# Optimization experiments

Hardware: AMD Instinct MI355X
Metric: run time of the kernel (lower is better)

Reference implementation:

```python
import jax, jax.numpy as jnp
import numpy as np

DIM = 1024
SCALE = 1.0 / np.sqrt(DIM).astype(np.float32)


def setup_inputs() -> dict:
    key = jax.random.key(0)
    ks = jax.random.split(key, 8)
    B, S, D = 4, 2048, DIM
    x = jax.random.normal(ks[0], (B, S, D), dtype=jnp.float32)
    mask = jnp.zeros((S, S), dtype=jnp.float32)  # additive mask, broadcast over batch
    # learned params (nn.Linear: y = x @ W.T + b); store W already transposed for x @ W
    init = 1.0 / np.sqrt(D)
    Wq = jax.random.uniform(ks[1], (D, D), jnp.float32, -init, init)
    bq = jax.random.uniform(ks[2], (D,), jnp.float32, -init, init)
    Wk = jax.random.uniform(ks[3], (D, D), jnp.float32, -init, init)
    bk = jax.random.uniform(ks[4], (D,), jnp.float32, -init, init)
    Wv = jax.random.uniform(ks[5], (D, D), jnp.float32, -init, init)
    bv = jax.random.uniform(ks[6], (D,), jnp.float32, -init, init)
    return {"x": x, "mask": mask, "Wq": Wq, "bq": bq, "Wk": Wk, "bk": bk, "Wv": Wv, "bv": bv}


def reference(x, mask, Wq, bq, Wk, bk, Wv, bv):
    # single-head full-dim attention, scaled by 1/sqrt(dim) (as in the source)
    q = x @ Wq + bq                      # [B, S, D]
    k = x @ Wk + bk                      # [B, S, D]
    v = x @ Wv + bv                      # [B, S, D]
    scores = jnp.einsum('bqd,bkd->bqk', q, k) * SCALE  # [B, S, S]
    scores = scores + mask               # additive mask, broadcast
    attn = jax.nn.softmax(scores, axis=-1)
    # dropout(p=0.1) is identity in eval mode
    return jnp.einsum('bqk,bkd->bqd', attn, v)  # [B, S, D]
```

## Files before the change

### kernel.cpp

```cpp
#include <hip/hip_runtime.h>

typedef unsigned short u16;
typedef unsigned int u32;

typedef __attribute__((ext_vector_type(8))) short bf16x8;
typedef __attribute__((ext_vector_type(4))) float f32x4;

static __device__ __forceinline__ u16 f2bf(float f) {
    u32 u = __float_as_uint(f);
    u32 r = (u + 0x7FFFu + ((u >> 16) & 1u)) >> 16;
    return (u16)r;
}
static __device__ __forceinline__ float bf2f(u16 h) {
    return __uint_as_float(((u32)h) << 16);
}
static __device__ __forceinline__ u32 pack2(float a, float b) {
    return (u32)f2bf(a) | ((u32)f2bf(b) << 16);
}

__global__ __launch_bounds__(256) void prep_kernel(
    const float* __restrict__ x, u16* __restrict__ xb,
    const float* __restrict__ mask, u16* __restrict__ maskb,
    const float* __restrict__ Wq, const float* __restrict__ Wk, const float* __restrict__ Wv,
    u16* __restrict__ T0, u16* __restrict__ T1, u16* __restrict__ T2,
    const float* __restrict__ bq, const float* __restrict__ bk,
    float* __restrict__ bqk, float* __restrict__ rsum) {
    const int D = 1024;
    int bid = blockIdx.x;
    const int tid = threadIdx.x;
    if (bid < 8192) {
        long i = (long)bid * 256 + tid;
        float4 v = ((const float4*)x)[i];
        ushort4 o; o.x = f2bf(v.x); o.y = f2bf(v.y); o.z = f2bf(v.z); o.w = f2bf(v.w);
        ((ushort4*)xb)[i] = o;
        return;
    }
    bid -= 8192;
    if (bid < 4096) {
        long i = (long)bid * 256 + tid;
        float4 v = ((const float4*)mask)[i];
        ushort4 o; o.x = f2bf(v.x); o.y = f2bf(v.y); o.z = f2bf(v.z); o.w = f2bf(v.w);
        ((ushort4*)maskb)[i] = o;
        return;
    }
    bid -= 4096;
    if (bid < 3072) {
        __shared__ float t[32][33];
        const int z = bid >> 10, loc = bid & 1023;
        const int bx = loc & 31, by = loc >> 5;
        const float* W = (z == 0) ? Wq : (z == 1) ? Wk : Wv;
        u16* WT = (z == 0) ? T0 : (z == 1) ? T1 : T2;
        const int tx = tid & 31, ty = tid >> 5;
#pragma unroll
        for (int i = ty; i < 32; i += 8)
            t[i][tx] = W[(long)(by * 32 + i) * D + bx * 32 + tx];
        __syncthreads();
#pragma unroll
        for (int i = ty; i < 32; i += 8)
            WT[(long)(bx * 32 + i) * D + by * 32 + tx] = f2bf(t[tx][i]);
        return;
    }
    bid -= 3072;
    if (bid < 8) {
        int i = bid * 256 + tid;
        bqk[i] = (i < 1024) ? bq[i] : bk[i - 1024];
        return;
    }
    bid -= 8;
    rsum[bid * 256 + tid] = 0.f;
}

static __device__ __forceinline__ void gemm_core(
    u16* __restrict__ SM,
    const u16* __restrict__ Ab, int lda,
    const u16* __restrict__ Bb, int ldb,
    void* __restrict__ Cb, int ldc, int c_bf16,
    const float* __restrict__ bias, int bias_mode,
    const u16* __restrict__ madd, int mask_ld,
    float* __restrict__ rowsum, int rs_mode,
    float scale, int K, int tm, int tn) {
    const int tid = threadIdx.x, wave = tid >> 6, lane = tid & 63;
    const int wm = (wave >> 1) * 64, wn = (wave & 1) * 64;
    const int lr = lane >> 2, c = lane & 3;
    const int fm = lane & 15, fq = lane >> 4;

    f32x4 acc[4][4];
#pragma unroll
    for (int i = 0; i < 4; i++)
#pragma unroll
        for (int j = 0; j < 4; j++) acc[i][j] = (f32x4){0.f, 0.f, 0.f, 0.f};

    const int T = K >> 5;

    auto stage = [&](int t, int buf) {
        u16* As = SM + buf * 8192;
        u16* Bs = As + 4096;
#pragma unroll
        for (int r = 0; r < 2; r++) {
            const int rl = r * 64 + wave * 16;
            const int row = rl + lr;
            const int kc = (t << 5) + ((c ^ ((row ^ (row >> 2)) & 3)) << 3);
            const u16* ga = Ab + (long)(tm + row) * lda + kc;
            const u16* gb = Bb + (long)(tn + row) * ldb + kc;
            __builtin_amdgcn_global_load_lds((const __attribute__((address_space(1))) void*)ga,
                                             (__attribute__((address_space(3))) void*)&As[rl * 32],
                                             16, 0, 0);
            __builtin_amdgcn_global_load_lds((const __attribute__((address_space(1))) void*)gb,
                                             (__attribute__((address_space(3))) void*)&Bs[rl * 32],
                                             16, 0, 0);
        }
    };

    stage(0, 0);
    __syncthreads();
    for (int t = 0; t < T; t++) {
        const int cur = t & 1;
        if (t + 1 < T) stage(t + 1, cur ^ 1);
        const u16* As = SM + cur * 8192;
        const u16* Bs = As + 4096;
        bf16x8 af[4], bfr[4];
#pragma unroll
        for (int i = 0; i < 4; i++) {
            int row = wm + i * 16 + fm;
            af[i] = *(const bf16x8*)&As[row * 32 + ((fq ^ ((row ^ (row >> 2)) & 3)) << 3)];
        }
#pragma unroll
        for (int j = 0; j < 4; j++) {
            int row = wn + j * 16 + fm;
            bfr[j] = *(const bf16x8*)&Bs[row * 32 + ((fq ^ ((row ^ (row >> 2)) & 3)) << 3)];
        }
#pragma unroll
        for (int i = 0; i < 4; i++)
#pragma unroll
            for (int j = 0; j < 4; j++)
                acc[i][j] = __builtin_amdgcn_mfma_f32_16x16x32_bf16(af[i], bfr[j], acc[i][j], 0, 0, 0);
        if (t + 1 < T) __syncthreads();
    }
    __syncthreads();

    float* EP = (float*)SM + wave * 1088;
    const int row16 = lane >> 2, cb = (lane & 3) * 16;
    float4 bc[4];
    if (bias_mode == 1) {
#pragma unroll
        for (int q = 0; q < 4; q++) bc[q] = *(const float4*)&bias[tn + wn + cb + q * 4];
    }
#pragma unroll
    for (int i = 0; i < 4; i++) {
#pragma unroll
        for (int j = 0; j < 4; j++)
#pragma unroll
            for (int r = 0; r < 4; r++)
                EP[(fq * 4 + r) * 68 + j * 16 + fm] = acc[i][j][r];
        const long grow = tm + wm + i * 16 + row16;
        float rb = (bias_mode == 2) ? bias[grow] : 0.f;
        float4 t4[4];
#pragma unroll
        for (int q = 0; q < 4; q++) {
            float4 v = *(const float4*)&EP[row16 * 68 + cb + q * 4];
            v.x = v.x * scale + rb; v.y = v.y * scale + rb;
            v.z = v.z * scale + rb; v.w = v.w * scale + rb;
            if (bias_mode == 1) { v.x += bc[q].x; v.y += bc[q].y; v.z += bc[q].z; v.w += bc[q].w; }
            if (madd) {
                ushort4 m4 = *(const ushort4*)&madd[grow * mask_ld + tn + wn + cb + q * 4];
                v.x += bf2f(m4.x); v.y += bf2f(m4.y); v.z += bf2f(m4.z); v.w += bf2f(m4.w);
            }
            t4[q] = v;
        }
        if (rs_mode == 1) {
            float s = 0.f;
#pragma unroll
            for (int q = 0; q < 4; q++) {
                t4[q].x = __expf(t4[q].x); t4[q].y = __expf(t4[q].y);
                t4[q].z = __expf(t4[q].z); t4[q].w = __expf(t4[q].w);
                s += t4[q].x + t4[q].y + t4[q].z + t4[q].w;
            }
            s += __shfl_xor(s, 1);
            s += __shfl_xor(s, 2);
            if ((lane & 3) == 0) atomicAdd(&rowsum[grow], s);
        } else if (rs_mode == 2) {
            float inv = 1.f / rowsum[grow];
#pragma unroll
            for (int q = 0; q < 4; q++) {
                t4[q].x *= inv; t4[q].y *= inv; t4[q].z *= inv; t4[q].w *= inv;
            }
        }
        if (c_bf16) {
            u16* dst = (u16*)Cb + grow * ldc + tn + wn + cb;
            uint4 o0 = {pack2(t4[0].x, t4[0].y), pack2(t4[0].z, t4[0].w),
                        pack2(t4[1].x, t4[1].y), pack2(t4[1].z, t4[1].w)};
            uint4 o1 = {pack2(t4[2].x, t4[2].y), pack2(t4[2].z, t4[2].w),
                        pack2(t4[3].x, t4[3].y), pack2(t4[3].z, t4[3].w)};
            *(uint4*)dst = o0;
            *(uint4*)(dst + 8) = o1;
        } else {
            float* dst = (float*)Cb + grow * ldc + tn + wn + cb;
#pragma unroll
            for (int q = 0; q < 4; q++) *(float4*)(dst + q * 4) = t4[q];
        }
    }
}

__global__ __launch_bounds__(256, 4) void gemm_qkvt_kernel(
    const u16* __restrict__ xb, const u16* __restrict__ wqkt, const u16* __restrict__ wvt,
    u16* __restrict__ QK, u16* __restrict__ VT,
    const float* __restrict__ bqk, const float* __restrict__ bv) {
    __shared__ __align__(16) u16 SM[2][256 * 32];
    const int D = 1024, MS = 8192;
    const int id = blockIdx.x;
    if (id < 1024) {
        gemm_core(&SM[0][0], xb, D, wqkt, D, QK, 2 * D, 1, bqk, 1, nullptr, 0,
                  nullptr, 0, 1.0f, D, (id >> 4) * 128, (id & 15) * 128);
    } else {
        const int f = id - 1024;
        gemm_core(&SM[0][0], wvt, D, xb, D, VT, MS, 1, bv, 2, nullptr, 0,
                  nullptr, 0, 1.0f, D, (f >> 6) * 128, (f & 63) * 128);
    }
}

__global__ __launch_bounds__(256, 4) void gemm_sc_kernel(
    const u16* __restrict__ QK, u16* __restrict__ sc,
    const u16* __restrict__ maskb, float* __restrict__ rsum, float scale) {
    __shared__ __align__(16) u16 SM[2][256 * 32];
    const int S = 2048, D = 1024;
    const int lin = blockIdx.x;
    const int xcd = lin & 7, r = lin >> 3;
    const int bx = r & 15, ylo = (r >> 4) & 7;
    const int bz = xcd >> 1, by = (xcd & 1) * 8 + ylo;
    gemm_core(&SM[0][0],
              QK + (long)bz * S * 2 * D, 2 * D,
              QK + D + (long)bz * S * 2 * D, 2 * D,
              sc + (long)bz * S * S, S, 1, nullptr, 0,
              maskb, S, rsum + (long)bz * S, 1,
              scale, D, by * 128, bx * 128);
}

__global__ __launch_bounds__(256, 4) void gemm_pv_kernel(
    const u16* __restrict__ sc, const u16* __restrict__ VT,
    float* __restrict__ out, const float* __restrict__ rsum) {
    __shared__ __align__(16) u16 SM[2][256 * 32];
    const int S = 2048, D = 1024, MS = 8192;
    const int xcd = blockIdx.x;
    const int s = blockIdx.y + 16 * blockIdx.z;
    const int bz = xcd >> 1;
    const int byi = (xcd & 1) * 8 + (s >> 3);
    const int bxi = s & 7;
    gemm_core(&SM[0][0],
              sc + (long)bz * S * S, S,
              VT + (long)bz * S, MS,
              out + (long)bz * S * D, D, 0, nullptr, 0,
              nullptr, 0, (float*)(rsum + (long)bz * S), 2,
              1.0f, S, byi * 128, bxi * 128);
}

extern "C" void kernel_launch(void* const* d_in, const int* in_sizes, int n_in,
                              void* d_out, int out_size, void* d_ws, size_t ws_size,
                              hipStream_t stream) {
    const float* x    = (const float*)d_in[0];
    const float* mask = (const float*)d_in[1];
    const float* Wq   = (const float*)d_in[2];
    const float* bq   = (const float*)d_in[3];
    const float* Wk   = (const float*)d_in[4];
    const float* bk   = (const float*)d_in[5];
    const float* Wv   = (const float*)d_in[6];
    const float* bv   = (const float*)d_in[7];
    float* out = (float*)d_out;

    const int B = 4, S = 2048, D = 1024;
    const long MS = (long)B * S;

    size_t need = (size_t)MS * D * 2 + (size_t)(2 * D) * D * 2 + (size_t)D * D * 2
                + (size_t)(2 * D) * 4 + (size_t)MS * (2 * D) * 2 + (size_t)D * MS * 2
                + (size_t)B * S * S * 2 + (size_t)B * S * 4 + (size_t)S * S * 2;
    if (ws_size < need) return;

    char* ws = (char*)d_ws;
    u16*  xb   = (u16*)ws;  ws += (long)MS * D * 2;
    u16*  wqkt = (u16*)ws;  ws += (long)(2 * D) * D * 2;
    u16*  wvt  = (u16*)ws;  ws += (long)D * D * 2;
    float* bqk = (float*)ws; ws += (long)(2 * D) * 4;
    u16*  QK   = (u16*)ws;  ws += (long)MS * (2 * D) * 2;
    u16*  VT   = (u16*)ws;  ws += (long)D * MS * 2;
    u16*  sc   = (u16*)ws;  ws += (long)B * S * S * 2;
    float* rsum = (float*)ws; ws += (long)B * S * 4;
    u16*  maskb = (u16*)ws; ws += (long)S * S * 2;

    const float SCALE = 0.03125f;

    prep_kernel<<<15400, 256, 0, stream>>>(x, xb, mask, maskb, Wq, Wk, Wv,
                                           wqkt, wqkt + (long)D * D, wvt,
                                           bq, bk, bqk, rsum);
    gemm_qkvt_kernel<<<1536, 256, 0, stream>>>(xb, wqkt, wvt, QK, VT, bqk, bv);
    gemm_sc_kernel<<<1024, 256, 0, stream>>>(QK, sc, maskb, rsum, SCALE);
    gemm_pv_kernel<<<dim3(8, 16, 4), 256, 0, stream>>>(sc, VT, out, rsum);
}
```

Before: 277.5 us.

## Load MFMA fragments directly from global memory in score and PV GEMMs

Replaces the LDS-staged, double-buffered GEMM main loop in the score and PV kernels with a register double-buffered loop that loads bf16x8 MFMA fragments straight from global memory. Each lane does per-row 16-byte loads that depend on L2/L1 for reuse, and occupancy hints drop to 2 blocks. The mask conversion and rowsum zeroing move out of the prep kernel into extra blocks of the QKV GEMM launch. This removes LDS traffic and barriers, but global loads become less coalesced and reuse across waves now depends on the cache hierarchy.

After: 417.0 us. 1.5x slower.

```diff
diff --git a/kernel.cpp b/kernel.cpp
--- a/kernel.cpp
+++ b/kernel.cpp
@@ -20,11 +20,10 @@
 
 __global__ __launch_bounds__(256) void prep_kernel(
     const float* __restrict__ x, u16* __restrict__ xb,
-    const float* __restrict__ mask, u16* __restrict__ maskb,
     const float* __restrict__ Wq, const float* __restrict__ Wk, const float* __restrict__ Wv,
     u16* __restrict__ T0, u16* __restrict__ T1, u16* __restrict__ T2,
     const float* __restrict__ bq, const float* __restrict__ bk,
-    float* __restrict__ bqk, float* __restrict__ rsum) {
+    float* __restrict__ bqk) {
     const int D = 1024;
     int bid = blockIdx.x;
     const int tid = threadIdx.x;
@@ -36,14 +35,6 @@
         return;
     }
     bid -= 8192;
-    if (bid < 4096) {
-        long i = (long)bid * 256 + tid;
-        float4 v = ((const float4*)mask)[i];
-        ushort4 o; o.x = f2bf(v.x); o.y = f2bf(v.y); o.z = f2bf(v.z); o.w = f2bf(v.w);
-        ((ushort4*)maskb)[i] = o;
-        return;
-    }
-    bid -= 4096;
     if (bid < 3072) {
         __shared__ float t[32][33];
         const int z = bid >> 10, loc = bid & 1023;
@@ -61,13 +52,10 @@
         return;
     }
     bid -= 3072;
-    if (bid < 8) {
+    {
         int i = bid * 256 + tid;
         bqk[i] = (i < 1024) ? bq[i] : bk[i - 1024];
-        return;
-    }
-    bid -= 8;
-    rsum[bid * 256 + tid] = 0.f;
+    }
 }
 
 static __device__ __forceinline__ void gemm_core(
@@ -76,8 +64,6 @@
     const u16* __restrict__ Bb, int ldb,
     void* __restrict__ Cb, int ldc, int c_bf16,
     const float* __restrict__ bias, int bias_mode,
-    const u16* __restrict__ madd, int mask_ld,
-    float* __restrict__ rowsum, int rs_mode,
     float scale, int K, int tm, int tn) {
     const int tid = threadIdx.x, wave = tid >> 6, lane = tid & 63;
     const int wm = (wave >> 1) * 64, wn = (wave & 1) * 64;
@@ -161,96 +147,201 @@
             v.x = v.x * scale + rb; v.y = v.y * scale + rb;
             v.z = v.z * scale + rb; v.w = v.w * scale + rb;
             if (bias_mode == 1) { v.x += bc[q].x; v.y += bc[q].y; v.z += bc[q].z; v.w += bc[q].w; }
-            if (madd) {
-                ushort4 m4 = *(const ushort4*)&madd[grow * mask_ld + tn + wn + cb + q * 4];
-                v.x += bf2f(m4.x); v.y += bf2f(m4.y); v.z += bf2f(m4.z); v.w += bf2f(m4.w);
-            }
             t4[q] = v;
         }
-        if (rs_mode == 1) {
-            float s = 0.f;
-#pragma unroll
-            for (int q = 0; q < 4; q++) {
-                t4[q].x = __expf(t4[q].x); t4[q].y = __expf(t4[q].y);
-                t4[q].z = __expf(t4[q].z); t4[q].w = __expf(t4[q].w);
-                s += t4[q].x + t4[q].y + t4[q].z + t4[q].w;
-            }
-            s += __shfl_xor(s, 1);
-            s += __shfl_xor(s, 2);
-            if ((lane & 3) == 0) atomicAdd(&rowsum[grow], s);
-        } else if (rs_mode == 2) {
-            float inv = 1.f / rowsum[grow];
-#pragma unroll
-            for (int q = 0; q < 4; q++) {
-                t4[q].x *= inv; t4[q].y *= inv; t4[q].z *= inv; t4[q].w *= inv;
-            }
-        }
-        if (c_bf16) {
-            u16* dst = (u16*)Cb + grow * ldc + tn + wn + cb;
-            uint4 o0 = {pack2(t4[0].x, t4[0].y), pack2(t4[0].z, t4[0].w),
-                        pack2(t4[1].x, t4[1].y), pack2(t4[1].z, t4[1].w)};
-            uint4 o1 = {pack2(t4[2].x, t4[2].y), pack2(t4[2].z, t4[2].w),
-                        pack2(t4[3].x, t4[3].y), pack2(t4[3].z, t4[3].w)};
-            *(uint4*)dst = o0;
-            *(uint4*)(dst + 8) = o1;
-        } else {
-            float* dst = (float*)Cb + grow * ldc + tn + wn + cb;
-#pragma unroll
-            for (int q = 0; q < 4; q++) *(float4*)(dst + q * 4) = t4[q];
-        }
+        u16* dst = (u16*)Cb + grow * ldc + tn + wn + cb;
+        uint4 o0 = {pack2(t4[0].x, t4[0].y), pack2(t4[0].z, t4[0].w),
+                    pack2(t4[1].x, t4[1].y), pack2(t4[1].z, t4[1].w)};
+        uint4 o1 = {pack2(t4[2].x, t4[2].y), pack2(t4[2].z, t4[2].w),
+                    pack2(t4[3].x, t4[3].y), pack2(t4[3].z, t4[3].w)};
+        *(uint4*)dst = o0;
+        *(uint4*)(dst + 8) = o1;
     }
 }
 
 __global__ __launch_bounds__(256, 4) void gemm_qkvt_kernel(
     const u16* __restrict__ xb, const u16* __restrict__ wqkt, const u16* __restrict__ wvt,
     u16* __restrict__ QK, u16* __restrict__ VT,
-    const float* __restrict__ bqk, const float* __restrict__ bv) {
+    const float* __restrict__ bqk, const float* __restrict__ bv,
+    const float* __restrict__ mask, u16* __restrict__ maskb, float* __restrict__ rsum) {
     __shared__ __align__(16) u16 SM[2][256 * 32];
     const int D = 1024, MS = 8192;
     const int id = blockIdx.x;
     if (id < 1024) {
-        gemm_core(&SM[0][0], xb, D, wqkt, D, QK, 2 * D, 1, bqk, 1, nullptr, 0,
-                  nullptr, 0, 1.0f, D, (id >> 4) * 128, (id & 15) * 128);
+        gemm_core(&SM[0][0], xb, D, wqkt, D, QK, 2 * D, 1, bqk, 1,
+                  1.0f, D, (id >> 4) * 128, (id & 15) * 128);
+    } else if (id < 1536) {
+        const int f = id - 1024;
+        gemm_core(&SM[0][0], wvt, D, xb, D, VT, MS, 1, bv, 2,
+                  1.0f, D, (f >> 6) * 128, (f & 63) * 128);
+    } else if (id < 5632) {
+        long i = (long)(id - 1536) * 256 + threadIdx.x;
+        float4 v = ((const float4*)mask)[i];
+        ushort4 o; o.x = f2bf(v.x); o.y = f2bf(v.y); o.z = f2bf(v.z); o.w = f2bf(v.w);
+        ((ushort4*)maskb)[i] = o;
     } else {
-        const int f = id - 1024;
-        gemm_core(&SM[0][0], wvt, D, xb, D, VT, MS, 1, bv, 2, nullptr, 0,
-                  nullptr, 0, 1.0f, D, (f >> 6) * 128, (f & 63) * 128);
-    }
-}
-
-__global__ __launch_bounds__(256, 4) void gemm_sc_kernel(
+        rsum[(id - 5632) * 256 + threadIdx.x] = 0.f;
+    }
+}
+
+static __device__ __forceinline__ void gemm_direct_loop(
+    const u16* __restrict__ Ab, int lda,
+    const u16* __restrict__ Bb, int ldb,
+    int tm, int tn, int K, f32x4 (&acc)[4][4]) {
+    const int tid = threadIdx.x, wave = tid >> 6, lane = tid & 63;
+    const int wm = (wave >> 1) * 64, wn = (wave & 1) * 64;
+    const int fm = lane & 15, fq = lane >> 4;
+    const int T = K >> 5;
+
+    const u16* Ap = Ab + (long)(tm + wm + fm) * lda + fq * 8;
+    const u16* Bp = Bb + (long)(tn + wn + fm) * ldb + fq * 8;
+
+    bf16x8 a0[4], b0[4], a1[4], b1[4];
+#pragma unroll
+    for (int i = 0; i < 4; i++) {
+        a0[i] = *(const bf16x8*)(Ap + (long)i * 16 * lda);
+        b0[i] = *(const bf16x8*)(Bp + (long)i * 16 * ldb);
+    }
+    for (int t = 0; t < T; t += 2) {
+        if (t + 1 < T) {
+#pragma unroll
+            for (int i = 0; i < 4; i++) {
+                a1[i] = *(const bf16x8*)(Ap + (long)i * 16 * lda + (t + 1) * 32);
+                b1[i] = *(const bf16x8*)(Bp + (long)i * 16 * ldb + (t + 1) * 32);
+            }
+        }
+#pragma unroll
+        for (int i = 0; i < 4; i++)
+#pragma unroll
+            for (int j = 0; j < 4; j++)
+                acc[i][j] = __builtin_amdgcn_mfma_f32_16x16x32_bf16(a0[i], b0[j], acc[i][j], 0, 0, 0);
+        if (t + 2 < T) {
+#pragma unroll
+            for (int i = 0; i < 4; i++) {
+                a0[i] = *(const bf16x8*)(Ap + (long)i * 16 * lda + (t + 2) * 32);
+                b0[i] = *(const bf16x8*)(Bp + (long)i * 16 * ldb + (t + 2) * 32);
+            }
+        }
+        if (t + 1 < T) {
+#pragma unroll
+            for (int i = 0; i < 4; i++)
+#pragma unroll
+                for (int j = 0; j < 4; j++)
+                    acc[i][j] = __builtin_amdgcn_mfma_f32_16x16x32_bf16(a1[i], b1[j], acc[i][j], 0, 0, 0);
+        }
+    }
+}
+
+__global__ __launch_bounds__(256, 2) void sc_direct_kernel(
     const u16* __restrict__ QK, u16* __restrict__ sc,
     const u16* __restrict__ maskb, float* __restrict__ rsum, float scale) {
-    __shared__ __align__(16) u16 SM[2][256 * 32];
+    __shared__ __align__(16) float EPS[4 * 1088];
     const int S = 2048, D = 1024;
     const int lin = blockIdx.x;
     const int xcd = lin & 7, r = lin >> 3;
     const int bx = r & 15, ylo = (r >> 4) & 7;
     const int bz = xcd >> 1, by = (xcd & 1) * 8 + ylo;
-    gemm_core(&SM[0][0],
-              QK + (long)bz * S * 2 * D, 2 * D,
-              QK + D + (long)bz * S * 2 * D, 2 * D,
-              sc + (long)bz * S * S, S, 1, nullptr, 0,
-              maskb, S, rsum + (long)bz * S, 1,
-              scale, D, by * 128, bx * 128);
-}
-
-__global__ __launch_bounds__(256, 4) void gemm_pv_kernel(
+    const int tm = by * 128, tn = bx * 128;
+    const u16* Ab = QK + (long)bz * S * 2 * D;
+    const u16* Bb = Ab + D;
+    u16* Cb = sc + (long)bz * S * S;
+    float* rs = rsum + (long)bz * S;
+
+    f32x4 acc[4][4];
+#pragma unroll
+    for (int i = 0; i < 4; i++)
+#pragma unroll
+        for (int j = 0; j < 4; j++) acc[i][j] = (f32x4){0.f, 0.f, 0.f, 0.f};
+
+    gemm_direct_loop(Ab, 2 * D, Bb, 2 * D, tm, tn, D, acc);
+
+    const int tid = threadIdx.x, wave = tid >> 6, lane = tid & 63;
+    const int wm = (wave >> 1) * 64, wn = (wave & 1) * 64;
+    const int fm = lane & 15, fq = lane >> 4;
+    float* EP = EPS + wave * 1088;
+    const int row16 = lane >> 2, cb = (lane & 3) * 16;
+#pragma unroll
+    for (int i = 0; i < 4; i++) {
+#pragma unroll
+        for (int j = 0; j < 4; j++)
+#pragma unroll
+            for (int rr = 0; rr < 4; rr++)
+                EP[(fq * 4 + rr) * 68 + j * 16 + fm] = acc[i][j][rr];
+        const long grow = tm + wm + i * 16 + row16;
+        float4 t4[4];
+#pragma unroll
+        for (int q = 0; q < 4; q++) {
+            float4 v = *(const float4*)&EP[row16 * 68 + cb + q * 4];
+            ushort4 m4 = *(const ushort4*)&maskb[grow * S + tn + wn + cb + q * 4];
+            v.x = v.x * scale + bf2f(m4.x); v.y = v.y * scale + bf2f(m4.y);
+            v.z = v.z * scale + bf2f(m4.z); v.w = v.w * scale + bf2f(m4.w);
+            t4[q] = v;
+        }
+        float s = 0.f;
+#pragma unroll
+        for (int q = 0; q < 4; q++) {
+            t4[q].x = __expf(t4[q].x); t4[q].y = __expf(t4[q].y);
+            t4[q].z = __expf(t4[q].z); t4[q].w = __expf(t4[q].w);
+            s += t4[q].x + t4[q].y + t4[q].z + t4[q].w;
+        }
+        s += __shfl_xor(s, 1);
+        s += __shfl_xor(s, 2);
+        if ((lane & 3) == 0) atomicAdd(&rs[grow], s);
+        u16* dst = Cb + grow * S + tn + wn + cb;
+        uint4 o0 = {pack2(t4[0].x, t4[0].y), pack2(t4[0].z, t4[0].w),
+                    pack2(t4[1].x, t4[1].y), pack2(t4[1].z, t4[1].w)};
+        uint4 o1 = {pack2(t4[2].x, t4[2].y), pack2(t4[2].z, t4[2].w),
+                    pack2(t4[3].x, t4[3].y), pack2(t4[3].z, t4[3].w)};
+        *(uint4*)dst = o0;
+        *(uint4*)(dst + 8) = o1;
+    }
+}
+
+__global__ __launch_bounds__(256, 2) void pv_direct_kernel(
     const u16* __restrict__ sc, const u16* __restrict__ VT,
     float* __restrict__ out, const float* __restrict__ rsum) {
-    __shared__ __align__(16) u16 SM[2][256 * 32];
+    __shared__ __align__(16) float EPS[4 * 1088];
     const int S = 2048, D = 1024, MS = 8192;
     const int xcd = blockIdx.x;
-    const int s = blockIdx.y + 16 * blockIdx.z;
+    const int s = blockIdx.y + gridDim.y * blockIdx.z;
     const int bz = xcd >> 1;
     const int byi = (xcd & 1) * 8 + (s >> 3);
     const int bxi = s & 7;
-    gemm_core(&SM[0][0],
-              sc + (long)bz * S * S, S,
-              VT + (long)bz * S, MS,
-              out + (long)bz * S * D, D, 0, nullptr, 0,
-              nullptr, 0, (float*)(rsum + (long)bz * S), 2,
-              1.0f, S, byi * 128, bxi * 128);
+    const int tm = byi * 128, tn = bxi * 128;
+    const u16* Ab = sc + (long)bz * S * S;
+    const u16* Bb = VT + (long)bz * S;
+    const float* rs = rsum + (long)bz * S;
+
+    f32x4 acc[4][4];
+#pragma unroll
+    for (int i = 0; i < 4; i++)
+#pragma unroll
+        for (int j = 0; j < 4; j++) acc[i][j] = (f32x4){0.f, 0.f, 0.f, 0.f};
+
+    gemm_direct_loop(Ab, S, Bb, MS, tm, tn, S, acc);
+
+    const int tid = threadIdx.x, wave = tid >> 6, lane = tid & 63;
+    const int wm = (wave >> 1) * 64, wn = (wave & 1) * 64;
+    const int fm = lane & 15, fq = lane >> 4;
+    float* EP = EPS + wave * 1088;
+    const int row16 = lane >> 2, cb = (lane & 3) * 16;
+#pragma unroll
+    for (int i = 0; i < 4; i++) {
+#pragma unroll
+        for (int j = 0; j < 4; j++)
+#pragma unroll
+            for (int rr = 0; rr < 4; rr++)
+                EP[(fq * 4 + rr) * 68 + j * 16 + fm] = acc[i][j][rr];
+        const long grow = tm + wm + i * 16 + row16;
+        float inv = 1.f / rs[grow];
+        float* dst = out + (long)bz * S * D + grow * D + tn + wn + cb;
+#pragma unroll
+        for (int q = 0; q < 4; q++) {
+            float4 v = *(const float4*)&EP[row16 * 68 + cb + q * 4];
+            v.x *= inv; v.y *= inv; v.z *= inv; v.w *= inv;
+            *(float4*)(dst + q * 4) = v;
+        }
+    }
 }
 
 extern "C" void kernel_launch(void* const* d_in, const int* in_sizes, int n_in,
@@ -287,10 +378,10 @@
 
     const float SCALE = 0.03125f;
 
-    prep_kernel<<<15400, 256, 0, stream>>>(x, xb, mask, maskb, Wq, Wk, Wv,
-                                           wqkt, wqkt + (long)D * D, wvt,
-                                           bq, bk, bqk, rsum);
-    gemm_qkvt_kernel<<<1536, 256, 0, stream>>>(xb, wqkt, wvt, QK, VT, bqk, bv);
-    gemm_sc_kernel<<<1024, 256, 0, stream>>>(QK, sc, maskb, rsum, SCALE);
-    gemm_pv_kernel<<<dim3(8, 16, 4), 256, 0, stream>>>(sc, VT, out, rsum);
-}
+    prep_kernel<<<11272, 256, 0, stream>>>(x, xb, Wq, Wk, Wv,
+                                           wqkt, wqkt + (long)D * D, wvt, bq, bk, bqk);
+    gemm_qkvt_kernel<<<5664, 256, 0, stream>>>(xb, wqkt, wvt, QK, VT, bqk, bv,
+                                               mask, maskb, rsum);
+    sc_direct_kernel<<<1024, 256, 0, stream>>>(QK, sc, maskb, rsum, SCALE);
+    pv_direct_kernel<<<dim3(8, 16, 4), 256, 0, stream>>>(sc, VT, out, rsum);
+}
```
